# Kernel optimization log

Measured on AMD Instinct MI355X. Metric: run time of the kernel, lower is better.

Reference implementation:

```python
import jax, jax.numpy as jnp
import numpy as np

N, E, IN, H, NEX, NCAT = 100000, 1600000, 165, 128, 50, 3
EPS = 1e-5


def setup_inputs() -> dict:
    key = jax.random.key(0)
    ks = jax.random.split(key, 12)
    rn = lambda k, shp: (jax.random.normal(k, shp, jnp.float32) * 0.05)
    x = jax.random.normal(ks[0], (N, IN), jnp.float32)
    edge_index = jax.random.randint(ks[1], (2, E), 0, N, jnp.int32)
    inp = {
        'x': x, 'edge_index': edge_index,
        # GCN convs
        'W1': rn(ks[2], (IN, H)), 'b1': jnp.zeros((H,), jnp.float32),
        'W2': rn(ks[3], (H, H)), 'b2': jnp.zeros((H,), jnp.float32),
        # backbone BN (train-mode batch stats)
        'g1': jnp.ones((H,), jnp.float32), 'be1': jnp.zeros((H,), jnp.float32),
        'g2': jnp.ones((H,), jnp.float32), 'be2': jnp.zeros((H,), jnp.float32),
        # forward head
        'fW1': rn(ks[4], (H, H)), 'fb1': jnp.zeros((H,), jnp.float32),
        'fg1': jnp.ones((H,), jnp.float32), 'fbe1': jnp.zeros((H,), jnp.float32),
        'fW2': rn(ks[5], (H, H // 2)), 'fb2': jnp.zeros((H // 2,), jnp.float32),
        'fg2': jnp.ones((H // 2,), jnp.float32), 'fbe2': jnp.zeros((H // 2,), jnp.float32),
        'fW3': rn(ks[6], (H // 2, NEX)), 'fb3': jnp.zeros((NEX,), jnp.float32),
        # backward head
        'bW1': rn(ks[7], (H, H // 2)), 'bb1': jnp.zeros((H // 2,), jnp.float32),
        'bg1': jnp.ones((H // 2,), jnp.float32), 'bbe1': jnp.zeros((H // 2,), jnp.float32),
        'bW2': rn(ks[8], (H // 2, NCAT)), 'bb2': jnp.zeros((NCAT,), jnp.float32),
    }
    return inp


def _bn(h, g, b):
    # BatchNorm1d, training-mode stats (biased variance), dropout treated as identity
    m = h.mean(0)
    v = ((h - m) ** 2).mean(0)
    return (h - m) * jax.lax.rsqrt(v + EPS) * g + b


def _gcn(h, W, b, src, dst, dinv, n):
    h = h @ W                                   # [N, out]
    coef = (dinv[src] * dinv[dst])[:, None]     # sym-normalized edge weights
    msg = h[src] * coef                         # [E+N, out] gather
    out = jax.ops.segment_sum(msg, dst, num_segments=n)  # scatter-add
    return out + b


def reference(x, edge_index, W1, b1, W2, b2, g1, be1, g2, be2,
              fW1, fb1, fg1, fbe1, fW2, fb2, fg2, fbe2, fW3, fb3,
              bW1, bb1, bg1, bbe1, bW2, bb2):
    n = x.shape[0]
    loop = jnp.arange(n, dtype=edge_index.dtype)
    src = jnp.concatenate([edge_index[0], loop])  # add self-loops (PyG default)
    dst = jnp.concatenate([edge_index[1], loop])
    deg = jax.ops.segment_sum(jnp.ones(src.shape, x.dtype), dst, num_segments=n)
    dinv = jnp.where(deg > 0, jax.lax.rsqrt(jnp.maximum(deg, 1.0)), 0.0)

    h = jax.nn.relu(_bn(_gcn(x, W1, b1, src, dst, dinv, n), g1, be1))
    h = jax.nn.relu(_bn(_gcn(h, W2, b2, src, dst, dinv, n), g2, be2))
    emb = h

    f = jax.nn.relu(_bn(emb @ fW1 + fb1, fg1, fbe1))
    f = jax.nn.relu(_bn(f @ fW2 + fb2, fg2, fbe2))
    forward_logits = f @ fW3 + fb3

    bwd = jax.nn.relu(_bn(emb @ bW1 + bb1, bg1, bbe1))
    backward_logits = bwd @ bW2 + bb2

    return forward_logits, backward_logits, emb
```

## Files before the change

kernel.cpp:

```cpp
#include <hip/hip_runtime.h>
#include <stdint.h>

constexpr int NN = 100000;
constexpr int NE = 1600000;
constexpr int DIN = 165;
constexpr int PSZ = 12500;
constexpr int CAP = 48;

typedef __attribute__((ext_vector_type(8))) short bh8;
typedef __attribute__((ext_vector_type(4))) float f4;
typedef __attribute__((ext_vector_type(4))) float fx4;
typedef __attribute__((ext_vector_type(4))) int ix4;

__device__ inline unsigned short f2bf(float x) {
  union { float f; uint32_t u; } un; un.f = x;
  uint32_t u = un.u;
  return (unsigned short)((u + 0x7FFFu + ((u >> 16) & 1u)) >> 16);
}
__device__ inline float bf2f(unsigned short u) {
  union { uint32_t i; float f; } c; c.i = (uint32_t)u << 16; return c.f;
}
__device__ inline float bflo(uint32_t v) {
  union { uint32_t i; float f; } c; c.i = v << 16; return c.f;
}
__device__ inline float bfhi(uint32_t v) {
  union { uint32_t i; float f; } c; c.i = v & 0xffff0000u; return c.f;
}

__device__ inline f4 mfma16(bh8 a, bh8 b, f4 c) {
  return __builtin_amdgcn_mfma_f32_16x16x32_bf16(a, b, c, 0, 0, 0);
}

constexpr size_t OFF_DEG    = 0;
constexpr size_t OFF_STATS  = 400128;
constexpr size_t ZERO_BYTES = OFF_STATS + (size_t)5*64*256*4;
constexpr size_t OFF_DINV   = ZERO_BYTES;
constexpr size_t OFF_W1T    = OFF_DINV + 400128;
constexpr size_t OFF_W2T    = OFF_W1T + 128*192*2;
constexpr size_t OFF_FW1T   = OFF_W2T + 128*128*2;
constexpr size_t OFF_FW2T   = OFF_FW1T + 128*128*2;
constexpr size_t OFF_FW3T   = OFF_FW2T + 64*128*2;
constexpr size_t OFF_BW1T   = OFF_FW3T + 64*64*2;
constexpr size_t OFF_BW2T   = OFF_BW1T + 64*128*2;
constexpr size_t OFF_COL    = (OFF_BW2T + 16*64*2 + 255) & ~(size_t)255;
constexpr size_t OFF_BUF0   = (OFF_COL + (size_t)NN*CAP*4 + 255) & ~(size_t)255;
constexpr size_t OFF_BUF1   = OFF_BUF0 + (size_t)NN*128*2;
constexpr size_t OFF_BUF2   = OFF_BUF1 + (size_t)NN*128*2;

__global__ __launch_bounds__(256) void k_bfill(const int* __restrict__ srcv, const int* __restrict__ dstv,
                                               int* __restrict__ deg, int* __restrict__ colv) {
  int part = blockIdx.x & 7;
  int lo = part * PSZ, hi = lo + PSZ;
  const ix4* s4 = (const ix4*)srcv;
  const ix4* d4 = (const ix4*)dstv;
  constexpr int NQ = NE / 4;
  int stride = (gridDim.x >> 3) * 256;
#pragma unroll 2
  for (int q = (blockIdx.x >> 3) * 256 + threadIdx.x; q < NQ; q += stride) {
    ix4 dd = __builtin_nontemporal_load(d4 + q);
    ix4 ss = __builtin_nontemporal_load(s4 + q);
#pragma unroll
    for (int u = 0; u < 4; ++u) {
      int d = dd[u];
      if (d >= lo && d < hi) {
        int p = atomicAdd(&deg[d], 1);
        if (p < CAP) colv[d * CAP + p] = ss[u];
      }
    }
  }
}

__global__ __launch_bounds__(256) void k_prep(const float* __restrict__ W1, const float* __restrict__ W2,
                                              const float* __restrict__ fW1, const float* __restrict__ fW2,
                                              const float* __restrict__ fW3, const float* __restrict__ bW1,
                                              const float* __restrict__ bW2, char* __restrict__ wsb,
                                              const int* __restrict__ deg, float* __restrict__ dinv) {
  int b = blockIdx.x, t = threadIdx.x;
  if (b >= 308) {
    int i = (b - 308) * 256 + t;
    if (i < NN) dinv[i] = rsqrtf((float)(deg[i] + 1));
    return;
  }
  const float* src; unsigned short* dst; int K, C, Kpad, base;
  if (b < 96)       { src = W1;  dst = (unsigned short*)(wsb + OFF_W1T);  K = DIN; C = 128; Kpad = 192; base = b; }
  else if (b < 160) { src = W2;  dst = (unsigned short*)(wsb + OFF_W2T);  K = 128; C = 128; Kpad = 128; base = b - 96; }
  else if (b < 224) { src = fW1; dst = (unsigned short*)(wsb + OFF_FW1T); K = 128; C = 128; Kpad = 128; base = b - 160; }
  else if (b < 256) { src = fW2; dst = (unsigned short*)(wsb + OFF_FW2T); K = 128; C = 64;  Kpad = 128; base = b - 224; }
  else if (b < 272) { src = fW3; dst = (unsigned short*)(wsb + OFF_FW3T); K = 64;  C = 50;  Kpad = 64;  base = b - 256; }
  else if (b < 304) { src = bW1; dst = (unsigned short*)(wsb + OFF_BW1T); K = 128; C = 64;  Kpad = 128; base = b - 272; }
  else              { src = bW2; dst = (unsigned short*)(wsb + OFF_BW2T); K = 64;  C = 3;   Kpad = 64;  base = b - 304; }
  int idx = base * 256 + t;
  int c = idx / Kpad, k = idx - c * Kpad;
  float v = (c < C && k < K) ? src[k * C + c] : 0.f;
  dst[idx] = f2bf(v);
}

__global__ __launch_bounds__(256) void k_gx(const float* __restrict__ x,
                                            const unsigned short* __restrict__ W1T,
                                            unsigned short* __restrict__ out) {
  constexpr int KL = 200;
  __shared__ __attribute__((aligned(16))) unsigned short Alds[64 * KL];
  int tid = threadIdx.x;
  int lane = tid & 63, wave = tid >> 6;
  int lr = lane & 15, lk = (lane >> 4) * 8;
  int rowbase = blockIdx.x * 64;

  bh8 bw[2][6];
#pragma unroll
  for (int ct = 0; ct < 2; ++ct)
#pragma unroll
    for (int kt = 0; kt < 6; ++kt)
      bw[ct][kt] = *(const bh8*)&W1T[((wave * 2 + ct) * 16 + lr) * 192 + kt * 32 + lk];

  size_t slab = (size_t)rowbase * DIN;
  long rem = (long)NN * DIN - (long)slab;
  int lim4 = rem >= 10560 ? 2640 : (int)(rem >> 2);
  for (int z = tid; z < 64 * (192 - DIN); z += 256) {
    int r = z / (192 - DIN), k = DIN + (z - r * (192 - DIN));
    Alds[r * KL + k] = 0;
  }
  float4 regs[11];
#pragma unroll
  for (int i = 0; i < 11; ++i) {
    int idx4 = tid + i * 256;
    if (idx4 < lim4) regs[i] = *(const float4*)(x + slab + (size_t)idx4 * 4);
  }
#pragma unroll
  for (int i = 0; i < 11; ++i) {
    int idx4 = tid + i * 256;
    if (idx4 < lim4) {
      int e = idx4 * 4;
      int r = e / DIN, k = e - r * DIN;
      float vv[4] = {regs[i].x, regs[i].y, regs[i].z, regs[i].w};
#pragma unroll
      for (int j = 0; j < 4; ++j) {
        Alds[r * KL + k] = f2bf(vv[j]);
        if (++k == DIN) { k = 0; ++r; }
      }
    }
  }
  __syncthreads();

  f4 acc[4][2] = {};
  for (int kt = 0; kt < 6; ++kt) {
    bh8 a[4];
#pragma unroll
    for (int rt = 0; rt < 4; ++rt)
      a[rt] = *(const bh8*)&Alds[(rt * 16 + lr) * KL + kt * 32 + lk];
#pragma unroll
    for (int rt = 0; rt < 4; ++rt) {
      acc[rt][0] = mfma16(a[rt], bw[0][kt], acc[rt][0]);
      acc[rt][1] = mfma16(a[rt], bw[1][kt], acc[rt][1]);
    }
  }
#pragma unroll
  for (int ct = 0; ct < 2; ++ct) {
    int c = (wave * 2 + ct) * 16 + lr;
#pragma unroll
    for (int rt = 0; rt < 4; ++rt) {
      int gr0 = rowbase + rt * 16 + (lane >> 4) * 4;
#pragma unroll
      for (int rg = 0; rg < 4; ++rg) {
        int gr = gr0 + rg;
        if (gr < NN) out[(size_t)gr * 128 + c] = f2bf(acc[rt][ct][rg]);
      }
    }
  }
}

template <int KPAD, int CPAD, bool OUTBF>
__global__ __launch_bounds__(256) void k_gemm(const unsigned short* __restrict__ in, int K, int C,
                                              const float* __restrict__ bnstats,
                                              const float* __restrict__ gamma,
                                              const float* __restrict__ beta,
                                              const unsigned short* __restrict__ WT,
                                              const float* __restrict__ bias,
                                              void* __restrict__ out_, float* __restrict__ statsOut) {
  constexpr int KL = KPAD + 8;
  constexpr int NKT = KPAD / 32;
  constexpr int NCTW = (CPAD >= 64) ? CPAD / 64 : 1;
  __shared__ __attribute__((aligned(16))) unsigned short Alds[64 * KL];
  __shared__ float s_sum[128], s_sq[128], sss[256], red[256], red2[256];
  int tid = threadIdx.x;
  int lane = tid & 63, wave = tid >> 6;
  int lr = lane & 15, lk = (lane >> 4) * 8;
  int rowbase = blockIdx.x * 64;
  bool hasbn = gamma != nullptr;
  if (statsOut && tid < 128) { s_sum[tid] = 0.f; s_sq[tid] = 0.f; }

  bh8 bw[NCTW][NKT];
#pragma unroll
  for (int ct = 0; ct < NCTW; ++ct) {
    int cg = (CPAD >= 64) ? (wave * NCTW + ct) : 0;
#pragma unroll
    for (int kt = 0; kt < NKT; ++kt)
      bw[ct][kt] = *(const bh8*)&WT[(cg * 16 + lr) * KPAD + kt * 32 + lk];
  }

  if (hasbn) {
    int c = tid & 127, h = tid >> 7;
    const float* sp = bnstats + h * 32 * 256;
    float s = 0.f, q = 0.f;
#pragma unroll
    for (int k2 = 0; k2 < 32; ++k2) { s += sp[k2 * 256 + c]; q += sp[k2 * 256 + 128 + c]; }
    red[tid] = s; red2[tid] = q;
  }

  constexpr int NL = (64 * KPAD / 8) / 256;
  bh8 vv[NL];
#pragma unroll
  for (int i = 0; i < NL; ++i) {
    int idx8 = tid + i * 256;
    int r = idx8 / (KPAD / 8);
    int k = (idx8 - r * (KPAD / 8)) * 8;
    int gr = rowbase + r;
    vv[i] = (gr < NN) ? *(const bh8*)(in + (size_t)gr * KPAD + k) : bh8{};
  }

  if (hasbn) {
    __syncthreads();
    if (tid < 128) {
      float s = red[tid] + red[tid + 128];
      float q = red2[tid] + red2[tid + 128];
      float mean = s * (1.f / NN);
      float var = fmaxf(q * (1.f / NN) - mean * mean, 0.f);
      float gm = (tid < K) ? gamma[tid] : 1.f;
      float bt = (tid < K) ? beta[tid] : 0.f;
      float scale = gm * rsqrtf(var + 1e-5f);
      sss[tid] = scale;
      sss[128 + tid] = bt - mean * scale;
    }
    __syncthreads();
  }

#pragma unroll
  for (int i = 0; i < NL; ++i) {
    int idx8 = tid + i * 256;
    int r = idx8 / (KPAD / 8);
    int k = (idx8 - r * (KPAD / 8)) * 8;
    bh8 v = vv[i];
    if (hasbn) {
#pragma unroll
      for (int j = 0; j < 8; ++j) {
        float f = bf2f((unsigned short)v[j]);
        f = fmaxf(fmaf(f, sss[k + j], sss[128 + k + j]), 0.f);
        v[j] = (short)f2bf(f);
      }
    }
    *(bh8*)&Alds[r * KL + k] = v;
  }
  __syncthreads();

  if constexpr (CPAD >= 64) {
    f4 acc[4][NCTW] = {};
    for (int kt = 0; kt < NKT; ++kt) {
      bh8 a[4];
#pragma unroll
      for (int rt = 0; rt < 4; ++rt)
        a[rt] = *(const bh8*)&Alds[(rt * 16 + lr) * KL + kt * 32 + lk];
#pragma unroll
      for (int rt = 0; rt < 4; ++rt)
#pragma unroll
        for (int ct = 0; ct < NCTW; ++ct)
          acc[rt][ct] = mfma16(a[rt], bw[ct][kt], acc[rt][ct]);
    }
#pragma unroll
    for (int ct = 0; ct < NCTW; ++ct) {
      int c = (wave * NCTW + ct) * 16 + lr;
      float bv = (bias != nullptr && c < C) ? bias[c] : 0.f;
      float cs = 0.f, cq = 0.f;
#pragma unroll
      for (int rt = 0; rt < 4; ++rt) {
        int gr0 = rowbase + rt * 16 + (lane >> 4) * 4;
#pragma unroll
        for (int rg = 0; rg < 4; ++rg) {
          int gr = gr0 + rg;
          if (gr < NN && c < C) {
            float v = acc[rt][ct][rg] + bv;
            if (OUTBF) {
              unsigned short ub = f2bf(v);
              ((unsigned short*)out_)[(size_t)gr * C + c] = ub;
              v = bf2f(ub);
            } else {
              ((float*)out_)[(size_t)gr * C + c] = v;
            }
            cs += v; cq += v * v;
          }
        }
      }
      if (statsOut && c < C) { atomicAdd(&s_sum[c], cs); atomicAdd(&s_sq[c], cq); }
    }
  } else {
    f4 acc = {};
    for (int kt = 0; kt < NKT; ++kt) {
      bh8 a = *(const bh8*)&Alds[(wave * 16 + lr) * KL + kt * 32 + lk];
      acc = mfma16(a, bw[0][kt], acc);
    }
    int r0 = rowbase + wave * 16 + (lane >> 4) * 4;
    int c = lr;
#pragma unroll
    for (int rg = 0; rg < 4; ++rg) {
      int gr = r0 + rg;
      if (gr < NN && c < C) {
        float v = acc[rg] + ((bias != nullptr) ? bias[c] : 0.f);
        if (OUTBF) ((unsigned short*)out_)[(size_t)gr * C + c] = f2bf(v);
        else       ((float*)out_)[(size_t)gr * C + c] = v;
      }
    }
  }
  if (statsOut) {
    __syncthreads();
    int slot = blockIdx.x & 63;
    if (tid < 128) {
      atomicAdd(&statsOut[slot * 256 + tid], s_sum[tid]);
      atomicAdd(&statsOut[slot * 256 + 128 + tid], s_sq[tid]);
    }
  }
}

__global__ __launch_bounds__(256) void k_agg(const unsigned short* __restrict__ t, const int* __restrict__ colv,
                                             const int* __restrict__ deg,
                                             const float* __restrict__ dinv, unsigned short* __restrict__ out,
                                             float* __restrict__ stats) {
  __shared__ float rs[8][64], rq[8][64];
  int tid = threadIdx.x;
  int lane = tid & 63, wave = tid >> 6;
  int lg = lane >> 5;
  int l = lane & 31;
  int p = blockIdx.x & 7;
  int half = p >> 2;
  int sub = p & 3;
  int g = blockIdx.x >> 3;
  int node = g * 32 + sub * 8 + wave * 2 + lg;
  int cb = half * 64 + l * 2;
  float a0 = 0.f, a1 = 0.f;
  if (node < NN) {
    float di = dinv[node];
    uint32_t sv = *(const uint32_t*)(t + (size_t)node * 128 + cb);
    a0 = di * di * bflo(sv); a1 = di * di * bfhi(sv);
    int start = node * CAP;
    int len = min(deg[node], CAP);
    for (int j0 = 0; j0 < len; j0 += 32) {
      int cnt = min(len - j0, 32);
      int id = 0; float dv = 0.f;
      if (l < cnt) { id = colv[start + j0 + l]; dv = dinv[id]; }
      int j = 0;
      for (; j + 8 <= cnt; j += 8) {
        int s[8]; float c[8]; uint32_t v[8];
#pragma unroll
        for (int u = 0; u < 8; ++u) { s[u] = __shfl(id, j + u, 32); c[u] = __shfl(dv, j + u, 32) * di; }
#pragma unroll
        for (int u = 0; u < 8; ++u) v[u] = *(const uint32_t*)(t + (size_t)s[u] * 128 + cb);
#pragma unroll
        for (int u = 0; u < 8; ++u) { a0 = fmaf(c[u], bflo(v[u]), a0); a1 = fmaf(c[u], bfhi(v[u]), a1); }
      }
      for (; j < cnt; ++j) {
        int s = __shfl(id, j, 32);
        float c = __shfl(dv, j, 32) * di;
        uint32_t v = *(const uint32_t*)(t + (size_t)s * 128 + cb);
        a0 = fmaf(c, bflo(v), a0); a1 = fmaf(c, bfhi(v), a1);
      }
    }
    unsigned short u0 = f2bf(a0), u1 = f2bf(a1);
    uint32_t pack = (uint32_t)u0 | ((uint32_t)u1 << 16);
    __builtin_nontemporal_store(pack, (uint32_t*)(out + (size_t)node * 128 + cb));
    a0 = bf2f(u0); a1 = bf2f(u1);
  }
  int grp = wave * 2 + lg;
  rs[grp][l * 2] = a0; rs[grp][l * 2 + 1] = a1;
  rq[grp][l * 2] = a0 * a0; rq[grp][l * 2 + 1] = a1 * a1;
  __syncthreads();
  if (tid < 64) {
    float s = 0.f, q = 0.f;
#pragma unroll
    for (int k = 0; k < 8; ++k) { s += rs[k][tid]; q += rq[k][tid]; }
    int slot = blockIdx.x & 63;
    atomicAdd(&stats[slot * 256 + half * 64 + tid], s);
    atomicAdd(&stats[slot * 256 + 128 + half * 64 + tid], q);
  }
}

__global__ __launch_bounds__(256) void k_head(const unsigned short* __restrict__ a2h,
                                              const float* __restrict__ bnstats,
                                              const float* __restrict__ gamma,
                                              const float* __restrict__ beta,
                                              const unsigned short* __restrict__ FW1T,
                                              const unsigned short* __restrict__ BW1T,
                                              float* __restrict__ emb,
                                              unsigned short* __restrict__ f1,
                                              unsigned short* __restrict__ b1,
                                              float* __restrict__ statsF, float* __restrict__ statsB) {
  constexpr int KL = 136;
  __shared__ __attribute__((aligned(16))) unsigned short Elds[64 * KL];
  __shared__ float sF_sum[128], sF_sq[128], sB_sum[64], sB_sq[64], sss[256], red[256], red2[256];
  int tid = threadIdx.x;
  int lane = tid & 63, wave = tid >> 6;
  int lr = lane & 15, lk = (lane >> 4) * 8;
  int rowbase = blockIdx.x * 64;
  if (tid < 128) { sF_sum[tid] = 0.f; sF_sq[tid] = 0.f; }
  if (tid < 64)  { sB_sum[tid] = 0.f; sB_sq[tid] = 0.f; }

  bh8 bwF[2][4], bwB[4];
#pragma unroll
  for (int ct = 0; ct < 2; ++ct)
#pragma unroll
    for (int kt = 0; kt < 4; ++kt)
      bwF[ct][kt] = *(const bh8*)&FW1T[((wave * 2 + ct) * 16 + lr) * 128 + kt * 32 + lk];
#pragma unroll
  for (int kt = 0; kt < 4; ++kt)
    bwB[kt] = *(const bh8*)&BW1T[(wave * 16 + lr) * 128 + kt * 32 + lk];

  {
    int c = tid & 127, h = tid >> 7;
    const float* sp = bnstats + h * 32 * 256;
    float s = 0.f, q = 0.f;
#pragma unroll
    for (int k2 = 0; k2 < 32; ++k2) { s += sp[k2 * 256 + c]; q += sp[k2 * 256 + 128 + c]; }
    red[tid] = s; red2[tid] = q;
  }

  bh8 vv[4];
#pragma unroll
  for (int i = 0; i < 4; ++i) {
    int idx8 = tid + i * 256;
    int r = idx8 >> 4, k = (idx8 & 15) * 8;
    int gr = rowbase + r;
    vv[i] = (gr < NN) ? *(const bh8*)(a2h + (size_t)gr * 128 + k) : bh8{};
  }
  __syncthreads();
  if (tid < 128) {
    float s = red[tid] + red[tid + 128];
    float q = red2[tid] + red2[tid + 128];
    float mean = s * (1.f / NN);
    float var = fmaxf(q * (1.f / NN) - mean * mean, 0.f);
    float scale = gamma[tid] * rsqrtf(var + 1e-5f);
    sss[tid] = scale;
    sss[128 + tid] = beta[tid] - mean * scale;
  }
  __syncthreads();

#pragma unroll
  for (int i = 0; i < 4; ++i) {
    int idx8 = tid + i * 256;
    int r = idx8 >> 4, k = (idx8 & 15) * 8;
    int gr = rowbase + r;
    bh8 v = vv[i];
    float f[8];
#pragma unroll
    for (int j = 0; j < 8; ++j) {
      f[j] = fmaxf(fmaf(bf2f((unsigned short)v[j]), sss[k + j], sss[128 + k + j]), 0.f);
      v[j] = (short)f2bf(f[j]);
    }
    *(bh8*)&Elds[r * KL + k] = v;
    if (gr < NN) {
      fx4 o0 = {f[0], f[1], f[2], f[3]};
      fx4 o1 = {f[4], f[5], f[6], f[7]};
      __builtin_nontemporal_store(o0, (fx4*)(emb + (size_t)gr * 128 + k));
      __builtin_nontemporal_store(o1, (fx4*)(emb + (size_t)gr * 128 + k + 4));
    }
  }
  __syncthreads();

  f4 accF[4][2] = {};
  f4 accB[4] = {};
  for (int kt = 0; kt < 4; ++kt) {
    bh8 a[4];
#pragma unroll
    for (int rt = 0; rt < 4; ++rt)
      a[rt] = *(const bh8*)&Elds[(rt * 16 + lr) * KL + kt * 32 + lk];
#pragma unroll
    for (int rt = 0; rt < 4; ++rt) {
      accF[rt][0] = mfma16(a[rt], bwF[0][kt], accF[rt][0]);
      accF[rt][1] = mfma16(a[rt], bwF[1][kt], accF[rt][1]);
      accB[rt]    = mfma16(a[rt], bwB[kt],    accB[rt]);
    }
  }

#pragma unroll
  for (int ct = 0; ct < 2; ++ct) {
    int c = (wave * 2 + ct) * 16 + lr;
    float cs = 0.f, cq = 0.f;
#pragma unroll
    for (int rt = 0; rt < 4; ++rt) {
      int gr0 = rowbase + rt * 16 + (lane >> 4) * 4;
#pragma unroll
      for (int rg = 0; rg < 4; ++rg) {
        int gr = gr0 + rg;
        if (gr < NN) {
          unsigned short ub = f2bf(accF[rt][ct][rg]);
          f1[(size_t)gr * 128 + c] = ub;
          float v = bf2f(ub);
          cs += v; cq += v * v;
        }
      }
    }
    atomicAdd(&sF_sum[c], cs); atomicAdd(&sF_sq[c], cq);
  }
  {
    int c = wave * 16 + lr;
    float cs = 0.f, cq = 0.f;
#pragma unroll
    for (int rt = 0; rt < 4; ++rt) {
      int gr0 = rowbase + rt * 16 + (lane >> 4) * 4;
#pragma unroll
      for (int rg = 0; rg < 4; ++rg) {
        int gr = gr0 + rg;
        if (gr < NN) {
          unsigned short ub = f2bf(accB[rt][rg]);
          b1[(size_t)gr * 64 + c] = ub;
          float v = bf2f(ub);
          cs += v; cq += v * v;
        }
      }
    }
    atomicAdd(&sB_sum[c], cs); atomicAdd(&sB_sq[c], cq);
  }
  __syncthreads();
  int slot = blockIdx.x & 63;
  if (tid < 128) {
    atomicAdd(&statsF[slot * 256 + tid], sF_sum[tid]);
    atomicAdd(&statsF[slot * 256 + 128 + tid], sF_sq[tid]);
  } else if (tid < 192) {
    int c = tid - 128;
    atomicAdd(&statsB[slot * 256 + c], sB_sum[c]);
    atomicAdd(&statsB[slot * 256 + 128 + c], sB_sq[c]);
  }
}

extern "C" void kernel_launch(void* const* d_in, const int* in_sizes, int n_in,
                              void* d_out, int out_size, void* d_ws, size_t ws_size,
                              hipStream_t stream) {
  (void)in_sizes; (void)n_in; (void)out_size; (void)ws_size;
  const float* x   = (const float*)d_in[0];
  const int*   ei  = (const int*)d_in[1];
  const float* W1  = (const float*)d_in[2];
  const float* W2  = (const float*)d_in[4];
  const float* g1  = (const float*)d_in[6];
  const float* be1 = (const float*)d_in[7];
  const float* g2  = (const float*)d_in[8];
  const float* be2 = (const float*)d_in[9];
  const float* fW1 = (const float*)d_in[10];
  const float* fg1 = (const float*)d_in[12];
  const float* fbe1= (const float*)d_in[13];
  const float* fW2 = (const float*)d_in[14];
  const float* fg2 = (const float*)d_in[16];
  const float* fbe2= (const float*)d_in[17];
  const float* fW3 = (const float*)d_in[18];
  const float* fb3 = (const float*)d_in[19];
  const float* bW1 = (const float*)d_in[20];
  const float* bg1 = (const float*)d_in[22];
  const float* bbe1= (const float*)d_in[23];
  const float* bW2 = (const float*)d_in[24];
  const float* bb2 = (const float*)d_in[25];

  float* outp = (float*)d_out;
  float* fl  = outp;
  float* bl  = outp + (size_t)NN * 50;
  float* emb = outp + (size_t)NN * 53;

  char* wsb = (char*)d_ws;
  int*   deg    = (int*)(wsb + OFF_DEG);
  float* stats  = (float*)(wsb + OFF_STATS);
  float* dinv   = (float*)(wsb + OFF_DINV);
  const unsigned short* W1T  = (const unsigned short*)(wsb + OFF_W1T);
  const unsigned short* W2T  = (const unsigned short*)(wsb + OFF_W2T);
  const unsigned short* FW1T = (const unsigned short*)(wsb + OFF_FW1T);
  const unsigned short* FW2T = (const unsigned short*)(wsb + OFF_FW2T);
  const unsigned short* FW3T = (const unsigned short*)(wsb + OFF_FW3T);
  const unsigned short* BW1T = (const unsigned short*)(wsb + OFF_BW1T);
  const unsigned short* BW2T = (const unsigned short*)(wsb + OFF_BW2T);
  int*            colv = (int*)(wsb + OFF_COL);
  unsigned short* buf0 = (unsigned short*)(wsb + OFF_BUF0);
  unsigned short* buf1 = (unsigned short*)(wsb + OFF_BUF1);
  unsigned short* buf2 = (unsigned short*)(wsb + OFF_BUF2);
  unsigned short* b1   = buf2 + (size_t)NN * 64;

  const int GG = (NN + 63) / 64;
  const int GA = 25000;
  const int GP = 2048;

  hipMemsetAsync(d_ws, 0, ZERO_BYTES, stream);

  k_bfill<<<GP, 256, 0, stream>>>(ei, ei + NE, deg, colv);
  k_prep <<<699, 256, 0, stream>>>(W1, W2, fW1, fW2, fW3, bW1, bW2, wsb, deg, dinv);

  k_gx<<<GG, 256, 0, stream>>>(x, W1T, buf0);
  k_agg<<<GA, 256, 0, stream>>>(buf0, colv, deg, dinv, buf1, stats + 0 * 16384);

  k_gemm<128, 128, true><<<GG, 256, 0, stream>>>(buf1, 128, 128, stats + 0 * 16384, g1, be1,
                                                 W2T, nullptr, buf0, nullptr);
  k_agg<<<GA, 256, 0, stream>>>(buf0, colv, deg, dinv, buf1, stats + 1 * 16384);

  k_head<<<GG, 256, 0, stream>>>(buf1, stats + 1 * 16384, g2, be2, FW1T, BW1T, emb, buf0, b1,
                                 stats + 2 * 16384, stats + 3 * 16384);

  k_gemm<128, 64, true><<<GG, 256, 0, stream>>>(buf0, 128, 64, stats + 2 * 16384, fg1, fbe1,
                                                FW2T, nullptr, buf2, stats + 4 * 16384);
  k_gemm<64, 64, false><<<GG, 256, 0, stream>>>(buf2, 64, 50, stats + 4 * 16384, fg2, fbe2,
                                                FW3T, fb3, fl, nullptr);

  k_gemm<64, 16, false><<<GG, 256, 0, stream>>>(b1, 64, 3, stats + 3 * 16384, bg1, bbe1,
                                                BW2T, bb2, bl, nullptr);
}
```

Baseline: 366.0 us.

## Store GCN features in column-blocked layout for narrower aggregation gathers

The transformed feature matrix feeding each aggregation is now written as eight column blocks of 16 channels (each block contiguous across nodes), from both k_gx and the second-layer GEMM. The aggregation kernel is restructured so that each block handles one 16-channel slice for 32 nodes, with 8 lanes per node gathering 32-byte neighbor rows. This keeps each slice's working set (3.2 MB) small enough to stay cache-resident while blocks sharing a slice run together. The per-block BN statistics reduction switches to shuffles. In exchange, each neighbor list and its dinv values are read eight times instead of twice, and gathers become many small 32-byte transactions.

```diff
diff --git a/kernel.cpp b/kernel.cpp
--- a/kernel.cpp
+++ b/kernel.cpp
@@ -6,6 +6,7 @@
 constexpr int DIN = 165;
 constexpr int PSZ = 12500;
 constexpr int CAP = 48;
+constexpr size_t TBLK = (size_t)NN * 16;
 
 typedef __attribute__((ext_vector_type(8))) short bh8;
 typedef __attribute__((ext_vector_type(4))) float f4;
@@ -156,19 +157,20 @@
 #pragma unroll
   for (int ct = 0; ct < 2; ++ct) {
     int c = (wave * 2 + ct) * 16 + lr;
+    unsigned short* ob = out + (size_t)(c >> 4) * TBLK + (c & 15);
 #pragma unroll
     for (int rt = 0; rt < 4; ++rt) {
       int gr0 = rowbase + rt * 16 + (lane >> 4) * 4;
 #pragma unroll
       for (int rg = 0; rg < 4; ++rg) {
         int gr = gr0 + rg;
-        if (gr < NN) out[(size_t)gr * 128 + c] = f2bf(acc[rt][ct][rg]);
-      }
-    }
-  }
-}
-
-template <int KPAD, int CPAD, bool OUTBF>
+        if (gr < NN) ob[(size_t)gr * 16] = f2bf(acc[rt][ct][rg]);
+      }
+    }
+  }
+}
+
+template <int KPAD, int CPAD, bool OUTBF, bool BLKOUT>
 __global__ __launch_bounds__(256) void k_gemm(const unsigned short* __restrict__ in, int K, int C,
                                               const float* __restrict__ bnstats,
                                               const float* __restrict__ gamma,
@@ -279,7 +281,10 @@
             float v = acc[rt][ct][rg] + bv;
             if (OUTBF) {
               unsigned short ub = f2bf(v);
-              ((unsigned short*)out_)[(size_t)gr * C + c] = ub;
+              if (BLKOUT)
+                ((unsigned short*)out_)[(size_t)(c >> 4) * TBLK + (size_t)gr * 16 + (c & 15)] = ub;
+              else
+                ((unsigned short*)out_)[(size_t)gr * C + c] = ub;
               v = bf2f(ub);
             } else {
               ((float*)out_)[(size_t)gr * C + c] = v;
@@ -322,61 +327,60 @@
                                              const int* __restrict__ deg,
                                              const float* __restrict__ dinv, unsigned short* __restrict__ out,
                                              float* __restrict__ stats) {
-  __shared__ float rs[8][64], rq[8][64];
+  __shared__ float rs[4][16], rq[4][16];
   int tid = threadIdx.x;
   int lane = tid & 63, wave = tid >> 6;
-  int lg = lane >> 5;
-  int l = lane & 31;
-  int p = blockIdx.x & 7;
-  int half = p >> 2;
-  int sub = p & 3;
-  int g = blockIdx.x >> 3;
-  int node = g * 32 + sub * 8 + wave * 2 + lg;
-  int cb = half * 64 + l * 2;
-  float a0 = 0.f, a1 = 0.f;
-  if (node < NN) {
-    float di = dinv[node];
-    uint32_t sv = *(const uint32_t*)(t + (size_t)node * 128 + cb);
-    a0 = di * di * bflo(sv); a1 = di * di * bfhi(sv);
-    int start = node * CAP;
-    int len = min(deg[node], CAP);
-    for (int j0 = 0; j0 < len; j0 += 32) {
-      int cnt = min(len - j0, 32);
-      int id = 0; float dv = 0.f;
-      if (l < cnt) { id = colv[start + j0 + l]; dv = dinv[id]; }
-      int j = 0;
-      for (; j + 8 <= cnt; j += 8) {
-        int s[8]; float c[8]; uint32_t v[8];
-#pragma unroll
-        for (int u = 0; u < 8; ++u) { s[u] = __shfl(id, j + u, 32); c[u] = __shfl(dv, j + u, 32) * di; }
-#pragma unroll
-        for (int u = 0; u < 8; ++u) v[u] = *(const uint32_t*)(t + (size_t)s[u] * 128 + cb);
-#pragma unroll
-        for (int u = 0; u < 8; ++u) { a0 = fmaf(c[u], bflo(v[u]), a0); a1 = fmaf(c[u], bfhi(v[u]), a1); }
-      }
-      for (; j < cnt; ++j) {
-        int s = __shfl(id, j, 32);
-        float c = __shfl(dv, j, 32) * di;
-        uint32_t v = *(const uint32_t*)(t + (size_t)s * 128 + cb);
-        a0 = fmaf(c, bflo(v), a0); a1 = fmaf(c, bfhi(v), a1);
-      }
-    }
-    unsigned short u0 = f2bf(a0), u1 = f2bf(a1);
-    uint32_t pack = (uint32_t)u0 | ((uint32_t)u1 << 16);
-    __builtin_nontemporal_store(pack, (uint32_t*)(out + (size_t)node * 128 + cb));
-    a0 = bf2f(u0); a1 = bf2f(u1);
-  }
-  int grp = wave * 2 + lg;
-  rs[grp][l * 2] = a0; rs[grp][l * 2 + 1] = a1;
-  rq[grp][l * 2] = a0 * a0; rq[grp][l * 2 + 1] = a1 * a1;
+  int gi = tid >> 3;
+  int l = tid & 7;
+  int e8 = blockIdx.x & 7;
+  int node = (blockIdx.x >> 3) * 32 + gi;
+  const unsigned short* ts = t + (size_t)e8 * TBLK;
+  int co = l * 2;
+  float di = dinv[node];
+  uint32_t sv = *(const uint32_t*)(ts + (size_t)node * 16 + co);
+  float a0 = di * di * bflo(sv), a1 = di * di * bfhi(sv);
+  int start = node * CAP;
+  int len = min(deg[node], CAP);
+  int j0 = 0;
+  for (; j0 + 8 <= len; j0 += 8) {
+    int id = colv[start + j0 + l];
+    float dv = dinv[id];
+    int s[8]; float c[8]; uint32_t v[8];
+#pragma unroll
+    for (int u = 0; u < 8; ++u) { s[u] = __shfl(id, u, 8); c[u] = __shfl(dv, u, 8) * di; }
+#pragma unroll
+    for (int u = 0; u < 8; ++u) v[u] = *(const uint32_t*)(ts + (size_t)s[u] * 16 + co);
+#pragma unroll
+    for (int u = 0; u < 8; ++u) { a0 = fmaf(c[u], bflo(v[u]), a0); a1 = fmaf(c[u], bfhi(v[u]), a1); }
+  }
+  int rem = len - j0;
+  if (rem > 0) {
+    int id = 0; float dv = 0.f;
+    if (l < rem) { id = colv[start + j0 + l]; dv = dinv[id]; }
+    int s[8]; float c[8]; uint32_t v[8];
+#pragma unroll
+    for (int u = 0; u < 8; ++u) { s[u] = __shfl(id, u, 8); c[u] = __shfl(dv, u, 8) * di; }
+#pragma unroll
+    for (int u = 0; u < 8; ++u) if (u < rem) v[u] = *(const uint32_t*)(ts + (size_t)s[u] * 16 + co);
+#pragma unroll
+    for (int u = 0; u < 8; ++u) if (u < rem) { a0 = fmaf(c[u], bflo(v[u]), a0); a1 = fmaf(c[u], bfhi(v[u]), a1); }
+  }
+  unsigned short u0 = f2bf(a0), u1 = f2bf(a1);
+  uint32_t pack = (uint32_t)u0 | ((uint32_t)u1 << 16);
+  __builtin_nontemporal_store(pack, (uint32_t*)(out + (size_t)node * 128 + e8 * 16 + co));
+  a0 = bf2f(u0); a1 = bf2f(u1);
+  float s0 = a0, q0 = a0 * a0, s1 = a1, q1 = a1 * a1;
+  s0 += __shfl_xor(s0, 8);  q0 += __shfl_xor(q0, 8);  s1 += __shfl_xor(s1, 8);  q1 += __shfl_xor(q1, 8);
+  s0 += __shfl_xor(s0, 16); q0 += __shfl_xor(q0, 16); s1 += __shfl_xor(s1, 16); q1 += __shfl_xor(q1, 16);
+  s0 += __shfl_xor(s0, 32); q0 += __shfl_xor(q0, 32); s1 += __shfl_xor(s1, 32); q1 += __shfl_xor(q1, 32);
+  if (lane < 8) { rs[wave][l * 2] = s0; rs[wave][l * 2 + 1] = s1; rq[wave][l * 2] = q0; rq[wave][l * 2 + 1] = q1; }
   __syncthreads();
-  if (tid < 64) {
-    float s = 0.f, q = 0.f;
-#pragma unroll
-    for (int k = 0; k < 8; ++k) { s += rs[k][tid]; q += rq[k][tid]; }
+  if (tid < 16) {
+    float s = rs[0][tid] + rs[1][tid] + rs[2][tid] + rs[3][tid];
+    float q = rq[0][tid] + rq[1][tid] + rq[2][tid] + rq[3][tid];
     int slot = blockIdx.x & 63;
-    atomicAdd(&stats[slot * 256 + half * 64 + tid], s);
-    atomicAdd(&stats[slot * 256 + 128 + half * 64 + tid], q);
+    atomicAdd(&stats[slot * 256 + e8 * 16 + tid], s);
+    atomicAdd(&stats[slot * 256 + 128 + e8 * 16 + tid], q);
   }
 }
 
@@ -576,7 +580,7 @@
   unsigned short* b1   = buf2 + (size_t)NN * 64;
 
   const int GG = (NN + 63) / 64;
-  const int GA = 25000;
+  const int GA = (NN / 32) * 8;
   const int GP = 2048;
 
   hipMemsetAsync(d_ws, 0, ZERO_BYTES, stream);
@@ -587,18 +591,18 @@
   k_gx<<<GG, 256, 0, stream>>>(x, W1T, buf0);
   k_agg<<<GA, 256, 0, stream>>>(buf0, colv, deg, dinv, buf1, stats + 0 * 16384);
 
-  k_gemm<128, 128, true><<<GG, 256, 0, stream>>>(buf1, 128, 128, stats + 0 * 16384, g1, be1,
-                                                 W2T, nullptr, buf0, nullptr);
+  k_gemm<128, 128, true, true><<<GG, 256, 0, stream>>>(buf1, 128, 128, stats + 0 * 16384, g1, be1,
+                                                       W2T, nullptr, buf0, nullptr);
   k_agg<<<GA, 256, 0, stream>>>(buf0, colv, deg, dinv, buf1, stats + 1 * 16384);
 
   k_head<<<GG, 256, 0, stream>>>(buf1, stats + 1 * 16384, g2, be2, FW1T, BW1T, emb, buf0, b1,
                                  stats + 2 * 16384, stats + 3 * 16384);
 
-  k_gemm<128, 64, true><<<GG, 256, 0, stream>>>(buf0, 128, 64, stats + 2 * 16384, fg1, fbe1,
-                                                FW2T, nullptr, buf2, stats + 4 * 16384);
-  k_gemm<64, 64, false><<<GG, 256, 0, stream>>>(buf2, 64, 50, stats + 4 * 16384, fg2, fbe2,
-                                                FW3T, fb3, fl, nullptr);
-
-  k_gemm<64, 16, false><<<GG, 256, 0, stream>>>(b1, 64, 3, stats + 3 * 16384, bg1, bbe1,
-                                                BW2T, bb2, bl, nullptr);
-}
+  k_gemm<128, 64, true, false><<<GG, 256, 0, stream>>>(buf0, 128, 64, stats + 2 * 16384, fg1, fbe1,
+                                                       FW2T, nullptr, buf2, stats + 4 * 16384);
+  k_gemm<64, 64, false, false><<<GG, 256, 0, stream>>>(buf2, 64, 50, stats + 4 * 16384, fg2, fbe2,
+                                                       FW3T, fb3, fl, nullptr);
+
+  k_gemm<64, 16, false, false><<<GG, 256, 0, stream>>>(b1, 64, 3, stats + 3 * 16384, bg1, bbe1,
+                                                       BW2T, bb2, bl, nullptr);
+}
```

New measurement: 488.7 us. 33.5% more time.
